# Kernel optimization log

Hardware: AMD Instinct MI355X
Metric: run time of the kernel (lower is better)

The kernel has to match this reference:

```python
import jax, jax.numpy as jnp
import numpy as np

B, NPG, FANOUT = 32, 1024, 4       # graphs, nodes per graph, tree fan-out
H = 128                            # x_size == h_size
NUM_LAYERS = 4
A, BCAPS = 8, 8                    # TreeCaps a, b
DCC, N_CLASSES = 16, 50
ROUTING_ITER = 3
TYPE_VOCAB, TOKEN_VOCAB = 1000, 30000
EPS = 1e-10


def _build_forest():
    # parent of node i (i>0) is (i-1)//FANOUT; node 0 is root. Same tree per graph.
    child = np.arange(1, NPG)
    parent = (child - 1) // FANOUT
    pos = ((child - 1) % FANOUT).astype(np.float32)           # position in parent's mailbox
    cnt = np.bincount(parent, minlength=NPG).astype(np.float32)
    k = cnt[parent]                                           # child count of each edge's parent
    denom = np.maximum(k - 1.0, 1.0)
    lw = np.where(k == 1.0, 1.0, (k - 1.0 - pos) / denom).astype(np.float32)
    rw = np.where(k == 1.0, 0.0, pos / denom).astype(np.float32)
    offs = (np.arange(B) * NPG)[:, None]
    src = (child[None, :] + offs).reshape(-1).astype(np.int32)
    dst = (parent[None, :] + offs).reshape(-1).astype(np.int32)
    return src, dst, np.tile(lw, B), np.tile(rw, B), np.tile(cnt > 0, B)


def setup_inputs() -> dict:
    key = jax.random.key(0)
    ks = jax.random.split(key, 9)
    src, dst, lw, rw, has_children = _build_forest()
    N = B * NPG
    u = lambda k, s: jax.random.uniform(k, s, jnp.float32, -0.1, 0.1)
    return {
        "type_ids": jax.random.randint(ks[0], (N,), 0, TYPE_VOCAB, dtype=jnp.int32),
        "token_ids": jax.random.randint(ks[1], (N,), 0, TOKEN_VOCAB, dtype=jnp.int32),
        "src": jnp.asarray(src), "dst": jnp.asarray(dst),
        "lw": jnp.asarray(lw), "rw": jnp.asarray(rw),
        "has_children": jnp.asarray(has_children),
        "type_emb": jax.random.normal(ks[2], (TYPE_VOCAB, H - H // 2), jnp.float32),
        "token_emb": jax.random.normal(ks[3], (TOKEN_VOCAB, H // 2), jnp.float32),
        "W_left": u(ks[4], (NUM_LAYERS, H, H)),
        "W_right": u(ks[5], (NUM_LAYERS, H, H)),
        "W_top": u(ks[6], (NUM_LAYERS, H, H)),
        "b_conv": u(ks[7], (NUM_LAYERS, H)),
        "Wjm": 0.01 * jax.random.normal(ks[8], (A * H, DCC, N_CLASSES, NUM_LAYERS), jnp.float32),
    }


def squash(x, axis=-1):
    sq = jnp.sum(x * x, axis=axis, keepdims=True)
    return x * (sq / (1.0 + sq) / (jnp.sqrt(sq + EPS) + 1e-8))


def _vts_routing(uu):
    # uu: [NPG, H, L]  (one graph's primary capsules)
    l2 = jnp.sum(uu.reshape(NPG, -1) ** 2, axis=1)
    _, top_b = jax.lax.top_k(l2, BCAPS)
    u_i = jax.lax.stop_gradient(uu[top_b].reshape(-1, NUM_LAYERS))  # [BCAPS*H, L]
    _, top_a = jax.lax.top_k(l2, A)
    v_j = uu[top_a].reshape(-1, NUM_LAYERS)                         # [A*H, L]
    alpha = jnp.zeros((BCAPS * H, A * H), uu.dtype)
    for _ in range(ROUTING_ITER):
        alpha = alpha + u_i @ v_j.T
        beta = jax.nn.softmax(alpha, axis=-1)
        v_j = beta.T @ u_i
    return squash(v_j)                                              # [A*H, L]


def _dynamic_routing(SC, Wjm):
    # SC: [B, A*H, L], Wjm: [A*H, DCC, S, L]
    v = jnp.einsum('ncsm,bnm->bnsc', Wjm, SC)
    v_stop = jax.lax.stop_gradient(v)
    delta = jnp.zeros(SC.shape[:2] + (N_CLASSES,), SC.dtype)
    z = None
    for r in range(ROUTING_ITER):
        gamma = jax.nn.softmax(delta, axis=-1)
        vv = v if r == ROUTING_ITER - 1 else v_stop
        z = squash(jnp.einsum('bns,bnsc->bsc', gamma, vv))
        if r < ROUTING_ITER - 1:
            delta = delta + jnp.einsum('bnsc,bsc->bns', v_stop, z)
    return z                                                        # [B, S, DCC]


def reference(type_ids, token_ids, src, dst, lw, rw, has_children,
              type_emb, token_emb, W_left, W_right, W_top, b_conv, Wjm):
    h = jnp.concatenate([type_emb[type_ids], token_emb[token_ids]], axis=1)  # [N, H]
    N = h.shape[0]
    feats = []
    for l in range(NUM_LAYERS):
        ch = h[src]                                                 # [E, H] gather children
        msg = (ch @ W_left[l]) * lw[:, None] + (ch @ W_right[l]) * rw[:, None]
        children = jax.ops.segment_sum(msg, dst, num_segments=N)
        new_h = jax.nn.relu(children + h @ W_top[l] + b_conv[l][None, :])
        h = jnp.where(has_children[:, None], new_h, h)              # leaves keep old h
        feats.append(h)
    layer_feats = jnp.stack(feats, axis=-1)                         # [N, H, L]
    SC = jax.vmap(_vts_routing)(layer_feats.reshape(B, NPG, H, NUM_LAYERS))
    z = _dynamic_routing(SC, Wjm)
    logit = jnp.sqrt(jnp.sum(z * z, axis=-1) + EPS)                 # [B, S]
    return (logit, logit)
```

## Files before the change

### kernel.cpp

```cpp
#include <hip/hip_runtime.h>


#define BG      32
#define NPG     1024
#define HH      128
#define NLAY    4
#define INT_PG  256
#define M_INT   8192
#define NN      32768
#define EPG     1023
#define DCC     16
#define NS      50

__global__ void k_init(const int* __restrict__ tids, const int* __restrict__ kids,
                       const float* __restrict__ temb, const float* __restrict__ kemb,
                       float* __restrict__ hA, float* __restrict__ hB,
                       const float* __restrict__ Wjm, float* __restrict__ WT) {
  __shared__ float w[3200];
  int tid = threadIdx.x;
  if (blockIdx.x < 4096) {
    int idx = blockIdx.x * 256 + tid;
    int n = idx >> 5, c4 = idx & 31;
    float4 v;
    if (c4 < 16) v = *(const float4*)(temb + tids[n] * 64 + c4 * 4);
    else         v = *(const float4*)(kemb + kids[n] * 64 + (c4 - 16) * 4);
    *(float4*)(hA + n * 128 + c4 * 4) = v;
    if ((n & 1023) >= INT_PG)
      *(float4*)(hB + n * 128 + c4 * 4) = v;
  } else {
    int n = blockIdx.x - 4096;
    for (int i = tid; i < 3200; i += 256) w[i] = Wjm[n * 3200 + i];
    __syncthreads();
    for (int i = tid; i < 3200; i += 256) {
      int s = i >> 6, cm = i & 63;
      int cc = cm >> 2, m = cm & 3;
      WT[(s * 1024 + n) * 64 + cm] = w[(cc * NS + s) * 4 + m];
    }
  }
}

__global__ __launch_bounds__(256) void k_conv(
    const float* __restrict__ hp, float* __restrict__ hn,
    const int* __restrict__ src, const float* __restrict__ lw,
    const float* __restrict__ rw,
    const float* __restrict__ Wl, const float* __restrict__ Wr,
    const float* __restrict__ Wt, const float* __restrict__ bias,
    float* __restrict__ feat) {
  __shared__ float Ws[2][32][128];
  __shared__ float AsT[2][32][20];
  __shared__ float hlS[16][128];
  __shared__ float hrS[16][128];
  int tid = threadIdx.x;
  int tx = tid & 31, ty = tid >> 5;
  int rowBase = blockIdx.x * 16;
  int g = rowBase >> 8, plBase = rowBase & 255;
  int nodeBase = g * NPG + plBase;

  #pragma unroll
  for (int t = 0; t < 2; ++t) {
    int it = t * 256 + tid;
    int pw = it >> 5, c4 = it & 31;
    int pl = plBase + pw;
    float4 al = make_float4(0.f, 0.f, 0.f, 0.f);
    float4 ar = make_float4(0.f, 0.f, 0.f, 0.f);
    #pragma unroll
    for (int j = 0; j < 4; ++j) {
      int cc = 4 * pl + 1 + j;
      if (cc < NPG) {
        int e = g * EPG + cc - 1;
        int child = src[e];
        float lv = lw[e], rv = rw[e];
        float4 hv = *(const float4*)(hp + child * 128 + c4 * 4);
        al.x = fmaf(lv, hv.x, al.x); al.y = fmaf(lv, hv.y, al.y);
        al.z = fmaf(lv, hv.z, al.z); al.w = fmaf(lv, hv.w, al.w);
        ar.x = fmaf(rv, hv.x, ar.x); ar.y = fmaf(rv, hv.y, ar.y);
        ar.z = fmaf(rv, hv.z, ar.z); ar.w = fmaf(rv, hv.w, ar.w);
      }
    }
    *(float4*)&hlS[pw][c4 * 4] = al;
    *(float4*)&hrS[pw][c4 * 4] = ar;
  }
  __syncthreads();

  float acc[2][4] = {};
  int sr = tid >> 3, sc4 = (tid & 7) * 4;

  {
    float4 av = make_float4(0.f, 0.f, 0.f, 0.f);
    if (tid < 128) av = *(const float4*)&hlS[sr][sc4];
    const float* wsrc = Wl;
    int f0 = tid, f1 = tid + 256, f2 = tid + 512, f3 = tid + 768;
    float4 wv0 = *(const float4*)(wsrc + (f0 >> 5) * 128 + (f0 & 31) * 4);
    float4 wv1 = *(const float4*)(wsrc + (f1 >> 5) * 128 + (f1 & 31) * 4);
    float4 wv2 = *(const float4*)(wsrc + (f2 >> 5) * 128 + (f2 & 31) * 4);
    float4 wv3 = *(const float4*)(wsrc + (f3 >> 5) * 128 + (f3 & 31) * 4);
    if (tid < 128) {
      AsT[0][sc4 + 0][sr] = av.x; AsT[0][sc4 + 1][sr] = av.y;
      AsT[0][sc4 + 2][sr] = av.z; AsT[0][sc4 + 3][sr] = av.w;
    }
    *(float4*)&Ws[0][f0 >> 5][(f0 & 31) * 4] = wv0;
    *(float4*)&Ws[0][f1 >> 5][(f1 & 31) * 4] = wv1;
    *(float4*)&Ws[0][f2 >> 5][(f2 & 31) * 4] = wv2;
    *(float4*)&Ws[0][f3 >> 5][(f3 & 31) * 4] = wv3;
  }
  __syncthreads();

  for (int kc = 0; kc < 12; ++kc) {
    int cur = kc & 1, nxt = cur ^ 1;
    if (kc < 11) {
      int kc1 = kc + 1;
      int ssel = kc1 >> 2, kcol = (kc1 & 3) * 32;
      float4 av = make_float4(0.f, 0.f, 0.f, 0.f);
      if (tid < 128) {
        if (ssel == 0)      av = *(const float4*)&hlS[sr][kcol + sc4];
        else if (ssel == 1) av = *(const float4*)&hrS[sr][kcol + sc4];
        else                av = *(const float4*)(hp + (nodeBase + sr) * 128 + kcol + sc4);
      }
      const float* wsrc = ((ssel == 0) ? Wl : (ssel == 1) ? Wr : Wt) + kcol * 128;
      int f0 = tid, f1 = tid + 256, f2 = tid + 512, f3 = tid + 768;
      float4 wv0 = *(const float4*)(wsrc + (f0 >> 5) * 128 + (f0 & 31) * 4);
      float4 wv1 = *(const float4*)(wsrc + (f1 >> 5) * 128 + (f1 & 31) * 4);
      float4 wv2 = *(const float4*)(wsrc + (f2 >> 5) * 128 + (f2 & 31) * 4);
      float4 wv3 = *(const float4*)(wsrc + (f3 >> 5) * 128 + (f3 & 31) * 4);
      if (tid < 128) {
        AsT[nxt][sc4 + 0][sr] = av.x; AsT[nxt][sc4 + 1][sr] = av.y;
        AsT[nxt][sc4 + 2][sr] = av.z; AsT[nxt][sc4 + 3][sr] = av.w;
      }
      *(float4*)&Ws[nxt][f0 >> 5][(f0 & 31) * 4] = wv0;
      *(float4*)&Ws[nxt][f1 >> 5][(f1 & 31) * 4] = wv1;
      *(float4*)&Ws[nxt][f2 >> 5][(f2 & 31) * 4] = wv2;
      *(float4*)&Ws[nxt][f3 >> 5][(f3 & 31) * 4] = wv3;
    }
    #pragma unroll
    for (int kk = 0; kk < 32; ++kk) {
      float4 wv = *(float4*)&Ws[cur][kk][tx * 4];
      float2 av2 = *(float2*)&AsT[cur][kk][ty * 2];
      float aa[2] = {av2.x, av2.y};
      float ww[4] = {wv.x, wv.y, wv.z, wv.w};
      #pragma unroll
      for (int i = 0; i < 2; ++i)
        #pragma unroll
        for (int j = 0; j < 4; ++j)
          acc[i][j] = fmaf(aa[i], ww[j], acc[i][j]);
    }
    if (kc != 11) __syncthreads();
  }
  float4 bv = *(const float4*)(bias + tx * 4);
  float bb[4] = {bv.x, bv.y, bv.z, bv.w};
  #pragma unroll
  for (int i = 0; i < 2; ++i) {
    int r = ty * 2 + i;
    float4 o = make_float4(fmaxf(acc[i][0] + bb[0], 0.f),
                           fmaxf(acc[i][1] + bb[1], 0.f),
                           fmaxf(acc[i][2] + bb[2], 0.f),
                           fmaxf(acc[i][3] + bb[3], 0.f));
    *(float4*)(feat + (rowBase + r) * 128 + tx * 4) = o;
    *(float4*)(hn + (nodeBase + r) * 128 + tx * 4) = o;
  }
}

__global__ void k_l2(const float* __restrict__ h, const float* __restrict__ feat,
                     float* __restrict__ l2) {
  int wid = (blockIdx.x * 256 + threadIdx.x) >> 6;
  int lane = threadIdx.x & 63;
  int g = wid >> 10, local = wid & 1023;
  float s = 0.f;
  if (local >= INT_PG) {
    const float* p = h + wid * 128;
    float a = p[lane], b = p[lane + 64];
    s = (a * a + b * b) * 4.f;
  } else {
    int row = (g * INT_PG + local) * 128;
    #pragma unroll
    for (int l = 0; l < 4; ++l) {
      const float* p = feat + l * (M_INT * 128) + row;
      float a = p[lane], b = p[lane + 64];
      s += a * a + b * b;
    }
  }
  #pragma unroll
  for (int off = 32; off; off >>= 1) s += __shfl_down(s, off);
  if (lane == 0) l2[wid] = s;
}

__global__ __launch_bounds__(256) void k_topsel(const float* __restrict__ l2,
                                                const float* __restrict__ h,
                                                const float* __restrict__ feat,
                                                float* __restrict__ U,
                                                float* __restrict__ Vsum) {
  __shared__ int ssel[8];
  int g = blockIdx.x, tid = threadIdx.x;
  int lane = tid & 63;
  if (tid < 64) {
    unsigned long long kk[16];
    #pragma unroll
    for (int k = 0; k < 16; ++k) {
      int i = k * 64 + lane;
      unsigned vb = __float_as_uint(l2[g * 1024 + i]);
      kk[k] = ((unsigned long long)vb << 32) | (unsigned)(~i);
    }
    for (int r = 0; r < 8; ++r) {
      unsigned long long best = 0ULL;
      #pragma unroll
      for (int k = 0; k < 16; ++k) best = (kk[k] > best) ? kk[k] : best;
      #pragma unroll
      for (int off = 32; off; off >>= 1) {
        unsigned long long o = __shfl_down(best, off);
        best = (o > best) ? o : best;
      }
      best = __shfl(best, 0);
      if (lane == 0) ssel[r] = (int)(~(unsigned)(best & 0xffffffffu));
      #pragma unroll
      for (int k = 0; k < 16; ++k) if (kk[k] == best) kk[k] = 0ULL;
    }
  }
  __syncthreads();
  for (int t = 0; t < 4; ++t) {
    int idx = t * 256 + tid;
    int rank = idx >> 7, hh = idx & 127;
    int local = ssel[rank];
    float4 v;
    if (local >= INT_PG) {
      float x = h[(g * NPG + local) * 128 + hh];
      v = make_float4(x, x, x, x);
    } else {
      int row = (g * INT_PG + local) * 128 + hh;
      v.x = feat[row];
      v.y = feat[M_INT * 128 + row];
      v.z = feat[2 * M_INT * 128 + row];
      v.w = feat[3 * M_INT * 128 + row];
    }
    int o = g * 1024 + rank * 128 + hh;
    ((float4*)U)[o] = v;
    ((float4*)Vsum)[o] = v;
  }
}

__global__ __launch_bounds__(1024) void k_vtsA(const float* __restrict__ U,
                                               const float* __restrict__ Vsum,
                                               float* __restrict__ mw, float* __restrict__ sw) {
  __shared__ float4 Vs2[64 * 17];
  int g = blockIdx.x >> 4, rb = (blockIdx.x & 15) * 64;
  int tid = threadIdx.x, p = tid & 15, r = tid >> 4;
  Vs2[(tid & 63) * 17 + (tid >> 6)] = ((const float4*)Vsum)[g * 1024 + tid];
  __syncthreads();
  float4 u = ((const float4*)U)[g * 1024 + rb + r];
  float m = -3.4e38f;
  for (int i = 0; i < 64; ++i) {
    float4 v = Vs2[i * 17 + p];
    float a = u.x * v.x + u.y * v.y + u.z * v.z + u.w * v.w;
    m = fmaxf(m, a);
  }
  #pragma unroll
  for (int mk = 8; mk; mk >>= 1) m = fmaxf(m, __shfl_xor(m, mk));
  float s = 0.f;
  for (int i = 0; i < 64; ++i) {
    float4 v = Vs2[i * 17 + p];
    float a = u.x * v.x + u.y * v.y + u.z * v.z + u.w * v.w;
    s += __expf(a - m);
  }
  #pragma unroll
  for (int mk = 8; mk; mk >>= 1) s += __shfl_xor(s, mk);
  if (p == 0) {
    mw[g * 1024 + rb + r] = m;
    sw[g * 1024 + rb + r] = s;
  }
}

__global__ __launch_bounds__(1024) void k_vtsB(const float* __restrict__ U,
                                               float* __restrict__ Vsum,
                                               const float* __restrict__ mw,
                                               const float* __restrict__ sw,
                                               float* __restrict__ SCT, int last) {
  __shared__ float4 Us2[64 * 17];
  __shared__ float2 Ms2[64 * 17];
  int g = blockIdx.x >> 4, cb = (blockIdx.x & 15) * 64;
  int tid = threadIdx.x, p = tid & 15, q = tid >> 4;
  Us2[(tid & 63) * 17 + (tid >> 6)] = ((const float4*)U)[g * 1024 + tid];
  Ms2[(tid & 63) * 17 + (tid >> 6)] =
      make_float2(mw[g * 1024 + tid], 1.0f / sw[g * 1024 + tid]);
  __syncthreads();
  float4 v = ((const float4*)Vsum)[g * 1024 + cb + q];
  float4 acc = make_float4(0.f, 0.f, 0.f, 0.f);
  for (int i = 0; i < 64; ++i) {
    float4 uu = Us2[i * 17 + p];
    float2 st = Ms2[i * 17 + p];
    float a = uu.x * v.x + uu.y * v.y + uu.z * v.z + uu.w * v.w;
    float w = __expf(a - st.x) * st.y;
    acc.x = fmaf(w, uu.x, acc.x); acc.y = fmaf(w, uu.y, acc.y);
    acc.z = fmaf(w, uu.z, acc.z); acc.w = fmaf(w, uu.w, acc.w);
  }
  #pragma unroll
  for (int mk = 8; mk; mk >>= 1) {
    acc.x += __shfl_xor(acc.x, mk);
    acc.y += __shfl_xor(acc.y, mk);
    acc.z += __shfl_xor(acc.z, mk);
    acc.w += __shfl_xor(acc.w, mk);
  }
  if (p == 0) {
    float4 o = acc;
    int jc = cb + q;
    if (last) {
      float sq = o.x * o.x + o.y * o.y + o.z * o.z + o.w * o.w;
      float f = (sq / (1.f + sq)) / (sqrtf(sq + 1e-10f) + 1e-8f);
      ((float4*)SCT)[jc * 32 + g] = make_float4(o.x * f, o.y * f, o.z * f, o.w * f);
    } else {
      float4 w0 = ((const float4*)Vsum)[g * 1024 + jc];
      ((float4*)Vsum)[g * 1024 + jc] = make_float4(w0.x + o.x, w0.y + o.y,
                                                   w0.z + o.z, w0.w + o.w);
    }
  }
}

__global__ __launch_bounds__(256) void k_zsweep(const float* __restrict__ WT,
                                                const float* __restrict__ SCT,
                                                const float* __restrict__ gT,
                                                float* __restrict__ zpart, int it0) {
  int sb = blockIdx.x >> 4, nb = blockIdx.x & 15;
  int tid = threadIdx.x;
  int b = tid & 31, ch = tid >> 5;
  int n0 = nb * 64;
  const float4* wt = (const float4*)WT + (sb * 1024 + n0) * 16;
  const float4* sct = (const float4*)SCT + n0 * 32 + b;
  const float* gp = gT + (sb * 1024 + n0) * 32 + b;
  float a0 = 0.f, a1 = 0.f;
  #pragma unroll 8
  for (int nn = 0; nn < 64; ++nn) {
    float4 w0 = wt[nn * 16 + ch];
    float4 w1 = wt[nn * 16 + ch + 8];
    float4 s4 = sct[nn * 32];
    float gm = it0 ? (1.0f / 50.0f) : gp[nn * 32];
    float t0 = w0.x * s4.x + w0.y * s4.y + w0.z * s4.z + w0.w * s4.w;
    float t1 = w1.x * s4.x + w1.y * s4.y + w1.z * s4.z + w1.w * s4.w;
    a0 = fmaf(gm, t0, a0);
    a1 = fmaf(gm, t1, a1);
  }
  zpart[blockIdx.x * 512 + tid] = a0;
  zpart[blockIdx.x * 512 + 256 + tid] = a1;
}

__global__ void k_zred(const float* __restrict__ zpart, float* __restrict__ z,
                       float* __restrict__ out, int last) {
  __shared__ float sb_[256];
  __shared__ float fb[16];
  __shared__ float sqb[16];
  int tid = threadIdx.x;
  int idx = blockIdx.x * 256 + tid;
  int c = idx & 15;
  int sbk = (idx >> 4) % NS;
  int b = idx / (16 * NS);
  int lofs = (c < 8) ? (c * 32 + b) : (256 + (c - 8) * 32 + b);
  const float* zp = zpart + sbk * 16 * 512 + lofs;
  float s = 0.f;
  #pragma unroll
  for (int nb = 0; nb < 16; ++nb) s += zp[nb * 512];
  sb_[tid] = s;
  __syncthreads();
  if ((tid & 15) == 0) {
    float sq = 0.f;
    #pragma unroll
    for (int cc = 0; cc < 16; ++cc) sq += sb_[tid + cc] * sb_[tid + cc];
    float f = (sq / (1.f + sq)) / (sqrtf(sq + 1e-10f) + 1e-8f);
    fb[tid >> 4] = f;
    sqb[tid >> 4] = sq;
  }
  __syncthreads();
  z[idx] = s * fb[tid >> 4];
  if (last && (tid & 15) == 0) {
    float sq = sqb[tid >> 4], f = fb[tid >> 4];
    float lg = sqrtf(sq * f * f + 1e-10f);
    int pr = idx >> 4;
    out[pr] = lg;
    out[pr + 1600] = lg;
  }
}

__global__ __launch_bounds__(256) void k_dsweep(const float* __restrict__ WT,
                                                const float* __restrict__ SCT,
                                                const float* __restrict__ z,
                                                float* __restrict__ delta,
                                                float* __restrict__ gT, int first) {
  __shared__ float wl[50 * 64];
  __shared__ float4 scl[32];
  __shared__ float dtot[NS][32];
  __shared__ float mb[32], ib[32];
  int n = blockIdx.x;
  int tid = threadIdx.x;
  for (int i = tid; i < 3200; i += 256)
    wl[i] = WT[((i >> 6) * 1024 + n) * 64 + (i & 63)];
  if (tid < 32) scl[tid] = ((const float4*)SCT)[n * 32 + tid];
  __syncthreads();
  for (int idx = tid; idx < 1600; idx += 256) {
    int s = idx >> 5, b = idx & 31;
    const float4* wp = (const float4*)(wl + s * 64);
    const float4* zp = (const float4*)(z + (b * 50 + s) * 16);
    float4 z0 = zp[0], z1 = zp[1], z2 = zp[2], z3 = zp[3];
    float zs[16] = {z0.x, z0.y, z0.z, z0.w, z1.x, z1.y, z1.z, z1.w,
                    z2.x, z2.y, z2.z, z2.w, z3.x, z3.y, z3.z, z3.w};
    float4 y = make_float4(0.f, 0.f, 0.f, 0.f);
    #pragma unroll
    for (int c = 0; c < 16; ++c) {
      float4 w = wp[c];
      float zc = zs[c];
      y.x = fmaf(zc, w.x, y.x); y.y = fmaf(zc, w.y, y.y);
      y.z = fmaf(zc, w.z, y.z); y.w = fmaf(zc, w.w, y.w);
    }
    float4 sc = scl[b];
    float dd = sc.x * y.x + sc.y * y.y + sc.z * y.z + sc.w * y.w;
    float dt = first ? dd : (delta[(s * 1024 + n) * 32 + b] + dd);
    dtot[s][b] = dt;
    if (first) delta[(s * 1024 + n) * 32 + b] = dt;
  }
  __syncthreads();
  if (tid < 32) {
    float m = -3.4e38f;
    for (int s = 0; s < NS; ++s) m = fmaxf(m, dtot[s][tid]);
    float sum = 0.f;
    for (int s = 0; s < NS; ++s) sum += __expf(dtot[s][tid] - m);
    mb[tid] = m; ib[tid] = 1.0f / sum;
  }
  __syncthreads();
  for (int idx = tid; idx < 1600; idx += 256) {
    int s = idx >> 5, b = idx & 31;
    gT[(s * 1024 + n) * 32 + b] = __expf(dtot[s][b] - mb[b]) * ib[b];
  }
}

extern "C" void kernel_launch(void* const* d_in, const int* in_sizes, int n_in,
                              void* d_out, int out_size, void* d_ws, size_t ws_size,
                              hipStream_t stream) {
  const int*   type_ids  = (const int*)d_in[0];
  const int*   token_ids = (const int*)d_in[1];
  const int*   src       = (const int*)d_in[2];
  const float* lw        = (const float*)d_in[4];
  const float* rw        = (const float*)d_in[5];
  const float* temb      = (const float*)d_in[7];
  const float* kemb      = (const float*)d_in[8];
  const float* Wl        = (const float*)d_in[9];
  const float* Wr        = (const float*)d_in[10];
  const float* Wt        = (const float*)d_in[11];
  const float* bconv     = (const float*)d_in[12];
  const float* Wjm       = (const float*)d_in[13];
  float* out = (float*)d_out;
  char* wsb = (char*)d_ws;

  float* hA    = (float*)(wsb + 0);
  float* hB    = (float*)(wsb + 16777216);
  float* feat  = (float*)(wsb + 33554432);
  float* WT    = (float*)(wsb + 50331648);
  float* delta = (float*)(wsb + 63438848);
  float* gT    = (float*)(wsb + 69992448);
  float* z     = (float*)(wsb + 76546048);
  float* l2b   = (float*)(wsb + 76853248);
  float* U     = (float*)(wsb + 76984320);
  float* Vsum  = (float*)(wsb + 77508608);
  float* mw    = (float*)(wsb + 78032896);
  float* sw    = (float*)(wsb + 78163968);
  float* SCT   = (float*)(wsb + 78295040);
  float* zpart = (float*)(wsb + 78819328);

  k_init<<<5120, 256, 0, stream>>>(type_ids, token_ids, temb, kemb, hA, hB,
                                   Wjm, WT);

  for (int l = 0; l < NLAY; ++l) {
    const float* hp = (l & 1) ? hB : hA;
    float*       hn = (l & 1) ? hA : hB;
    k_conv<<<512, 256, 0, stream>>>(hp, hn, src, lw, rw,
                                    Wl + l * 16384, Wr + l * 16384, Wt + l * 16384,
                                    bconv + l * 128, feat + l * (M_INT * 128));
  }

  k_l2<<<8192, 256, 0, stream>>>(hA, feat, l2b);
  k_topsel<<<32, 256, 0, stream>>>(l2b, hA, feat, U, Vsum);

  for (int it = 0; it < 3; ++it) {
    k_vtsA<<<512, 1024, 0, stream>>>(U, Vsum, mw, sw);
    k_vtsB<<<512, 1024, 0, stream>>>(U, Vsum, mw, sw, SCT, it == 2 ? 1 : 0);
  }

  for (int it = 0; it < 3; ++it) {
    k_zsweep<<<800, 256, 0, stream>>>(WT, SCT, gT, zpart, it == 0 ? 1 : 0);
    k_zred<<<100, 256, 0, stream>>>(zpart, z, out, it == 2 ? 1 : 0);
    if (it < 2)
      k_dsweep<<<1024, 256, 0, stream>>>(WT, SCT, z, delta, gT, it == 0 ? 1 : 0);
  }
}
```

Baseline: 433.2 us.

## Single-buffer conv tiles in shared memory and split z-sweep into more blocks

The conv GEMM drops its double-buffered shared-memory tiles for a single buffer guarded by two barriers per k-chunk. This lowers LDS use per block so more blocks can be resident, but it gives up the overlap of global loads with compute. The z-sweep now splits each class over 32 node chunks instead of 16, doubling the block count for more parallelism. The reduction kernel sums twice as many partials, and the partial buffer must be large enough for the doubled layout.

```diff
diff --git a/kernel.cpp b/kernel.cpp
--- a/kernel.cpp
+++ b/kernel.cpp
@@ -46,8 +46,8 @@
     const float* __restrict__ Wl, const float* __restrict__ Wr,
     const float* __restrict__ Wt, const float* __restrict__ bias,
     float* __restrict__ feat) {
-  __shared__ float Ws[2][32][128];
-  __shared__ float AsT[2][32][20];
+  __shared__ float Ws[32][128];
+  __shared__ float AsT[32][20];
   __shared__ float hlS[16][128];
   __shared__ float hrS[16][128];
   int tid = threadIdx.x;
@@ -85,56 +85,40 @@
   float acc[2][4] = {};
   int sr = tid >> 3, sc4 = (tid & 7) * 4;
 
-  {
+  for (int kc = 0; kc < 12; ++kc) {
+    int ssel = kc >> 2, kcol = (kc & 3) * 32;
     float4 av = make_float4(0.f, 0.f, 0.f, 0.f);
-    if (tid < 128) av = *(const float4*)&hlS[sr][sc4];
-    const float* wsrc = Wl;
-    int f0 = tid, f1 = tid + 256, f2 = tid + 512, f3 = tid + 768;
-    float4 wv0 = *(const float4*)(wsrc + (f0 >> 5) * 128 + (f0 & 31) * 4);
-    float4 wv1 = *(const float4*)(wsrc + (f1 >> 5) * 128 + (f1 & 31) * 4);
-    float4 wv2 = *(const float4*)(wsrc + (f2 >> 5) * 128 + (f2 & 31) * 4);
-    float4 wv3 = *(const float4*)(wsrc + (f3 >> 5) * 128 + (f3 & 31) * 4);
     if (tid < 128) {
-      AsT[0][sc4 + 0][sr] = av.x; AsT[0][sc4 + 1][sr] = av.y;
-      AsT[0][sc4 + 2][sr] = av.z; AsT[0][sc4 + 3][sr] = av.w;
-    }
-    *(float4*)&Ws[0][f0 >> 5][(f0 & 31) * 4] = wv0;
-    *(float4*)&Ws[0][f1 >> 5][(f1 & 31) * 4] = wv1;
-    *(float4*)&Ws[0][f2 >> 5][(f2 & 31) * 4] = wv2;
-    *(float4*)&Ws[0][f3 >> 5][(f3 & 31) * 4] = wv3;
-  }
-  __syncthreads();
-
-  for (int kc = 0; kc < 12; ++kc) {
-    int cur = kc & 1, nxt = cur ^ 1;
-    if (kc < 11) {
-      int kc1 = kc + 1;
-      int ssel = kc1 >> 2, kcol = (kc1 & 3) * 32;
-      float4 av = make_float4(0.f, 0.f, 0.f, 0.f);
-      if (tid < 128) {
-        if (ssel == 0)      av = *(const float4*)&hlS[sr][kcol + sc4];
-        else if (ssel == 1) av = *(const float4*)&hrS[sr][kcol + sc4];
-        else                av = *(const float4*)(hp + (nodeBase + sr) * 128 + kcol + sc4);
-      }
-      const float* wsrc = ((ssel == 0) ? Wl : (ssel == 1) ? Wr : Wt) + kcol * 128;
+      if (ssel == 0)      av = *(const float4*)&hlS[sr][kcol + sc4];
+      else if (ssel == 1) av = *(const float4*)&hrS[sr][kcol + sc4];
+      else                av = *(const float4*)(hp + (nodeBase + sr) * 128 + kcol + sc4);
+    }
+    const float* wsrc = ((ssel == 0) ? Wl : (ssel == 1) ? Wr : Wt) + kcol * 128;
+    float4 wv0, wv1, wv2, wv3;
+    {
       int f0 = tid, f1 = tid + 256, f2 = tid + 512, f3 = tid + 768;
-      float4 wv0 = *(const float4*)(wsrc + (f0 >> 5) * 128 + (f0 & 31) * 4);
-      float4 wv1 = *(const float4*)(wsrc + (f1 >> 5) * 128 + (f1 & 31) * 4);
-      float4 wv2 = *(const float4*)(wsrc + (f2 >> 5) * 128 + (f2 & 31) * 4);
-      float4 wv3 = *(const float4*)(wsrc + (f3 >> 5) * 128 + (f3 & 31) * 4);
-      if (tid < 128) {
-        AsT[nxt][sc4 + 0][sr] = av.x; AsT[nxt][sc4 + 1][sr] = av.y;
-        AsT[nxt][sc4 + 2][sr] = av.z; AsT[nxt][sc4 + 3][sr] = av.w;
-      }
-      *(float4*)&Ws[nxt][f0 >> 5][(f0 & 31) * 4] = wv0;
-      *(float4*)&Ws[nxt][f1 >> 5][(f1 & 31) * 4] = wv1;
-      *(float4*)&Ws[nxt][f2 >> 5][(f2 & 31) * 4] = wv2;
-      *(float4*)&Ws[nxt][f3 >> 5][(f3 & 31) * 4] = wv3;
-    }
+      wv0 = *(const float4*)(wsrc + (f0 >> 5) * 128 + (f0 & 31) * 4);
+      wv1 = *(const float4*)(wsrc + (f1 >> 5) * 128 + (f1 & 31) * 4);
+      wv2 = *(const float4*)(wsrc + (f2 >> 5) * 128 + (f2 & 31) * 4);
+      wv3 = *(const float4*)(wsrc + (f3 >> 5) * 128 + (f3 & 31) * 4);
+    }
+    __syncthreads();
+    if (tid < 128) {
+      AsT[sc4 + 0][sr] = av.x; AsT[sc4 + 1][sr] = av.y;
+      AsT[sc4 + 2][sr] = av.z; AsT[sc4 + 3][sr] = av.w;
+    }
+    {
+      int f0 = tid, f1 = tid + 256, f2 = tid + 512, f3 = tid + 768;
+      *(float4*)&Ws[f0 >> 5][(f0 & 31) * 4] = wv0;
+      *(float4*)&Ws[f1 >> 5][(f1 & 31) * 4] = wv1;
+      *(float4*)&Ws[f2 >> 5][(f2 & 31) * 4] = wv2;
+      *(float4*)&Ws[f3 >> 5][(f3 & 31) * 4] = wv3;
+    }
+    __syncthreads();
     #pragma unroll
     for (int kk = 0; kk < 32; ++kk) {
-      float4 wv = *(float4*)&Ws[cur][kk][tx * 4];
-      float2 av2 = *(float2*)&AsT[cur][kk][ty * 2];
+      float4 wv = *(float4*)&Ws[kk][tx * 4];
+      float2 av2 = *(float2*)&AsT[kk][ty * 2];
       float aa[2] = {av2.x, av2.y};
       float ww[4] = {wv.x, wv.y, wv.z, wv.w};
       #pragma unroll
@@ -143,7 +127,6 @@
         for (int j = 0; j < 4; ++j)
           acc[i][j] = fmaf(aa[i], ww[j], acc[i][j]);
     }
-    if (kc != 11) __syncthreads();
   }
   float4 bv = *(const float4*)(bias + tx * 4);
   float bb[4] = {bv.x, bv.y, bv.z, bv.w};
@@ -316,16 +299,16 @@
                                                 const float* __restrict__ SCT,
                                                 const float* __restrict__ gT,
                                                 float* __restrict__ zpart, int it0) {
-  int sb = blockIdx.x >> 4, nb = blockIdx.x & 15;
+  int sb = blockIdx.x >> 5, nb = blockIdx.x & 31;
   int tid = threadIdx.x;
   int b = tid & 31, ch = tid >> 5;
-  int n0 = nb * 64;
+  int n0 = nb * 32;
   const float4* wt = (const float4*)WT + (sb * 1024 + n0) * 16;
   const float4* sct = (const float4*)SCT + n0 * 32 + b;
   const float* gp = gT + (sb * 1024 + n0) * 32 + b;
   float a0 = 0.f, a1 = 0.f;
   #pragma unroll 8
-  for (int nn = 0; nn < 64; ++nn) {
+  for (int nn = 0; nn < 32; ++nn) {
     float4 w0 = wt[nn * 16 + ch];
     float4 w1 = wt[nn * 16 + ch + 8];
     float4 s4 = sct[nn * 32];
@@ -350,10 +333,10 @@
   int sbk = (idx >> 4) % NS;
   int b = idx / (16 * NS);
   int lofs = (c < 8) ? (c * 32 + b) : (256 + (c - 8) * 32 + b);
-  const float* zp = zpart + sbk * 16 * 512 + lofs;
+  const float* zp = zpart + sbk * 32 * 512 + lofs;
   float s = 0.f;
   #pragma unroll
-  for (int nb = 0; nb < 16; ++nb) s += zp[nb * 512];
+  for (int nb = 0; nb < 32; ++nb) s += zp[nb * 512];
   sb_[tid] = s;
   __syncthreads();
   if ((tid & 15) == 0) {
@@ -479,7 +462,7 @@
   }
 
   for (int it = 0; it < 3; ++it) {
-    k_zsweep<<<800, 256, 0, stream>>>(WT, SCT, gT, zpart, it == 0 ? 1 : 0);
+    k_zsweep<<<1600, 256, 0, stream>>>(WT, SCT, gT, zpart, it == 0 ? 1 : 0);
     k_zred<<<100, 256, 0, stream>>>(zpart, z, out, it == 2 ? 1 : 0);
     if (it < 2)
       k_dsweep<<<1024, 256, 0, stream>>>(WT, SCT, z, delta, gT, it == 0 ? 1 : 0);
```

New measurement: 431.2 us. No clear change (-0.5%).
